# Kernel tuning notes

Hardware: AMD Instinct MI355X
Metric: run time of the kernel (lower is better)

Reference implementation:

```python
import jax, jax.numpy as jnp
import numpy as np
import math

N, C_S, C_Z, C_IPA, H, NQ, NV = 768, 384, 128, 16, 12, 4, 8


def setup_inputs() -> dict:
    key = jax.random.key(0)
    ks = jax.random.split(key, 16)
    inp = {
        "s": jax.random.normal(ks[0], (N, C_S), jnp.float32),
        "z": jax.random.normal(ks[1], (N, N, C_Z), jnp.float32),
        "rots": jax.random.normal(ks[2], (N, 3, 3), jnp.float32),
        "trans": jax.random.normal(ks[3], (N, 3), jnp.float32),
        "mask": jnp.ones((N,), jnp.float32),
    }
    sc = 0.02
    inp["Wq"] = jax.random.normal(ks[4], (C_S, H * C_IPA), jnp.float32) * sc
    inp["bq"] = jnp.zeros((H * C_IPA,), jnp.float32)
    inp["Wkv"] = jax.random.normal(ks[5], (C_S, H * 2 * C_IPA), jnp.float32) * sc
    inp["bkv"] = jnp.zeros((H * 2 * C_IPA,), jnp.float32)
    inp["Wq3"] = jax.random.normal(ks[6], (C_S, H * 3 * NQ), jnp.float32) * sc
    inp["bq3"] = jnp.zeros((H * 3 * NQ,), jnp.float32)
    inp["Wkv3"] = jax.random.normal(ks[7], (C_S, H * 3 * (NQ + NV)), jnp.float32) * sc
    inp["bkv3"] = jnp.zeros((H * 3 * (NQ + NV),), jnp.float32)
    inp["Wb"] = jax.random.normal(ks[8], (C_Z, H), jnp.float32) * sc
    inp["bb"] = jnp.zeros((H,), jnp.float32)
    inp["hw"] = jnp.zeros((H,), jnp.float32)
    inp["Wo"] = jax.random.normal(ks[9], (H * (C_Z + C_IPA + NV * 4), C_S), jnp.float32) * sc
    inp["bo"] = jnp.zeros((C_S,), jnp.float32)
    return inp


def reference(s, z, rots, trans, mask, Wq, bq, Wkv, bkv, Wq3, bq3, Wkv3, bkv3, Wb, bb, hw, Wo, bo):
    normsize = math.sqrt(1.0 / (3 * C_IPA))
    normsize_B = math.sqrt(1.0 / 3.0)
    normsize_hw = math.sqrt(1.0 / (3 * NQ * 9.0 / 2))

    # scalar Q/K/V: [N, H, C_IPA]
    Q = (s @ Wq + bq).reshape(N, H, C_IPA)
    KV = (s @ Wkv + bkv).reshape(N, H, 2, C_IPA)
    K, V = KV[..., 0, :], KV[..., 1, :]

    # query points: project, place into global frame via rigid transform
    Q3 = (s @ Wq3 + bq3).reshape(N, 3, NQ * H).swapaxes(-1, -2)        # [N, NQ*H, 3]
    Q3 = jnp.einsum('nij,nkj->nki', rots, Q3) + trans[:, None, :]
    Q3 = Q3.reshape(N, H, NQ, 3)

    KV3 = (s @ Wkv3 + bkv3).reshape(N, 3, H * (NQ + NV)).swapaxes(-1, -2)
    KV3 = jnp.einsum('nij,nkj->nki', rots, KV3) + trans[:, None, :]
    KV3 = KV3.reshape(N, H, NQ + NV, 3)
    K3, V3 = KV3[:, :, :NQ, :], KV3[:, :, NQ:, :]                      # points per head

    # pair bias [N, N, H]
    B = z @ Wb + bb

    # scalar attention logits + pair bias
    AT = jnp.einsum('ihc,jhc->ijh', Q, K) * normsize + B * normsize_B

    # point attention: squared distances [N, N, H, NQ]
    d2 = jnp.sum(jnp.square(Q3[:, None] - K3[None, :]), axis=-1)
    hw_sp = jax.nn.softplus(hw) * normsize_hw                          # [H]
    AT3 = -0.5 * jnp.sum(d2 * hw_sp[None, None, :, None], axis=-1)     # [N, N, H]

    # mask bias: large negative where either residue masked out
    mask2 = mask[:, None] * mask[None, :]
    B3 = (mask2 - 1.0) * 1e9                                           # [N, N]

    AT = jax.nn.softmax(AT + AT3 + B3[..., None], axis=-2)             # softmax over j

    # scalar value aggregation
    O = jnp.einsum('ijh,jhc->ihc', AT, V).reshape(N, -1)

    # point value aggregation, then map back to local frame (inverse transform)
    O3 = jnp.einsum('ijh,jhcd->ihcd', AT, V3).reshape(N, H * NV, 3)
    O3 = jnp.einsum('nji,nkj->nki', rots, O3 - trans[:, None, :])      # rots^T @ (O3 - t)
    O3_norm = jnp.sqrt(jnp.sum(jnp.square(O3), axis=-1) + 1e-20)       # [N, H*NV]

    # pair representation aggregation
    O_pair = jnp.einsum('ijh,ijc->ihc', AT, z).reshape(N, -1)

    O_final = jnp.concatenate((O, O3[..., 0], O3[..., 1], O3[..., 2], O3_norm, O_pair), axis=-1)
    return O_final @ Wo + bo
```

## Files before the change

kernel.cpp:

```cpp
#include <hip/hip_runtime.h>
#include <cstdint>


typedef __attribute__((ext_vector_type(8))) short short8;
typedef __attribute__((ext_vector_type(4))) short short4_t;
typedef __attribute__((ext_vector_type(4))) float f32x4;

__device__ __forceinline__ unsigned short f2bf(float f) {
    unsigned u = __float_as_uint(f);
    u = (u + 0x7FFFu + ((u >> 16) & 1u)) >> 16;
    return (unsigned short)u;
}
__device__ __forceinline__ float bf2f(unsigned short s) {
    return __uint_as_float(((unsigned)s) << 16);
}
__device__ __forceinline__ unsigned pk2(float lo, float hi) {
    return (unsigned)f2bf(lo) | ((unsigned)f2bf(hi) << 16);
}
__device__ __forceinline__ int HOFF(int gg) {
    return gg * 6 + ((gg & 2) << 2);
}

#define NS_QK  0.14433756729740643f
#define NS_B   0.5773502691896258f
#define NS_HW  0.13608276348795434f

__global__ __launch_bounds__(256) void proj_kernel(
    const float* __restrict__ s,
    const float* __restrict__ Wq,   const float* __restrict__ bq,
    const float* __restrict__ Wkv,  const float* __restrict__ bkv,
    const float* __restrict__ Wq3,  const float* __restrict__ bq3,
    const float* __restrict__ Wkv3, const float* __restrict__ bkv3,
    float* __restrict__ Qw, unsigned short* __restrict__ Kw,
    unsigned short* __restrict__ Vt,
    float* __restrict__ P3q, float* __restrict__ P3kv)
{
    __shared__ __align__(16) float s_lds[32 * 384];
    const int t  = threadIdx.x;
    const int r0 = blockIdx.x * 32;
    const int c0 = blockIdx.y * 128;

    for (int u = t; u < 3072; u += 256) {
        int r = u / 96, c4 = u - r * 96;
        *(float4*)&s_lds[r * 384 + c4 * 4] =
            *(const float4*)&s[(size_t)(r0 + r) * 384 + c4 * 4];
    }
    __syncthreads();

    const int rg = t >> 6;
    const int lc = t & 63;
    const int colA = c0 + lc;
    const int colB = c0 + lc + 64;

    const float *wpA, *wpB; int ldA, ldB; float biasA, biasB;
    {
        int col = colA;
        if (col < 192)      { wpA = Wq   + col;       ldA = 192; biasA = bq[col]; }
        else if (col < 576) { wpA = Wkv  + (col-192); ldA = 384; biasA = bkv[col-192]; }
        else if (col < 720) { wpA = Wq3  + (col-576); ldA = 144; biasA = bq3[col-576]; }
        else                { wpA = Wkv3 + (col-720); ldA = 432; biasA = bkv3[col-720]; }
        col = colB;
        if (col < 192)      { wpB = Wq   + col;       ldB = 192; biasB = bq[col]; }
        else if (col < 576) { wpB = Wkv  + (col-192); ldB = 384; biasB = bkv[col-192]; }
        else if (col < 720) { wpB = Wq3  + (col-576); ldB = 144; biasB = bq3[col-576]; }
        else                { wpB = Wkv3 + (col-720); ldB = 432; biasB = bkv3[col-720]; }
    }

    float acc0[8] = {}, acc1[8] = {};
    for (int k = 0; k < 384; k += 4) {
        float4 sv[8];
        #pragma unroll
        for (int r = 0; r < 8; r++)
            sv[r] = *(const float4*)&s_lds[(rg*8 + r) * 384 + k];
        #pragma unroll
        for (int kk = 0; kk < 4; kk++) {
            float w0 = wpA[(k + kk) * ldA];
            float w1 = wpB[(k + kk) * ldB];
            #pragma unroll
            for (int r = 0; r < 8; r++) {
                float sval = ((const float*)&sv[r])[kk];
                acc0[r] += sval * w0;
                acc1[r] += sval * w1;
            }
        }
    }

    #pragma unroll
    for (int q = 0; q < 2; q++) {
        int col   = q ? colB : colA;
        float bia = q ? biasB : biasA;
        #pragma unroll
        for (int r = 0; r < 8; r++) {
            int row = r0 + rg*8 + r;
            float v = (q ? acc1[r] : acc0[r]) + bia;
            if (col < 192) {
                Qw[(size_t)row*192 + col] = v;
            } else if (col < 576) {
                int c = col - 192, h = c >> 5, sub = c & 31;
                if (sub < 16) Kw[(size_t)row*192 + h*16 + sub] = f2bf(v);
                else          Vt[(size_t)(h*16 + (sub-16))*768 + row] = f2bf(v);
            } else if (col < 720) {
                P3q[(size_t)row*144 + (col-576)] = v;
            } else {
                P3kv[(size_t)row*432 + (col-720)] = v;
            }
        }
    }
}

__global__ __launch_bounds__(192) void rot3_kernel(
    const float* __restrict__ P3q, const float* __restrict__ P3kv,
    const float* __restrict__ rots, const float* __restrict__ trans,
    float* __restrict__ Q3w, float* __restrict__ K3w,
    unsigned short* __restrict__ V3t)
{
    const int n = blockIdx.x;
    const int t = threadIdx.x;
    float R[9];
    #pragma unroll
    for (int u = 0; u < 9; u++) R[u] = rots[n*9 + u];
    float T0 = trans[n*3+0], T1 = trans[n*3+1], T2 = trans[n*3+2];

    float p0, p1, p2;
    if (t < 48) {
        p0 = P3q[(size_t)n*144 + t];
        p1 = P3q[(size_t)n*144 + 48 + t];
        p2 = P3q[(size_t)n*144 + 96 + t];
    } else {
        int k = t - 48;
        p0 = P3kv[(size_t)n*432 + k];
        p1 = P3kv[(size_t)n*432 + 144 + k];
        p2 = P3kv[(size_t)n*432 + 288 + k];
    }
    float o0 = R[0]*p0 + R[1]*p1 + R[2]*p2 + T0;
    float o1 = R[3]*p0 + R[4]*p1 + R[5]*p2 + T1;
    float o2 = R[6]*p0 + R[7]*p1 + R[8]*p2 + T2;

    if (t < 48) {
        Q3w[(size_t)n*144 + t*3 + 0] = o0;
        Q3w[(size_t)n*144 + t*3 + 1] = o1;
        Q3w[(size_t)n*144 + t*3 + 2] = o2;
    } else {
        int k = t - 48, h = k / 12, m = k % 12;
        if (m < 4) {
            size_t base = (size_t)n*144 + (h*4 + m)*3;
            K3w[base+0] = o0; K3w[base+1] = o1; K3w[base+2] = o2;
        } else {
            int rv = (h*8 + (m-4))*3;
            V3t[(size_t)(rv+0)*768 + n] = f2bf(o0);
            V3t[(size_t)(rv+1)*768 + n] = f2bf(o1);
            V3t[(size_t)(rv+2)*768 + n] = f2bf(o2);
        }
    }
}

__global__ __launch_bounds__(256) void ek_kernel(
    const float* __restrict__ Qw, const unsigned short* __restrict__ Kw,
    const float* __restrict__ Q3w, const float* __restrict__ K3w,
    const float* __restrict__ mask, const float* __restrict__ hw,
    const float* __restrict__ bb,
    unsigned short* __restrict__ EQw, unsigned short* __restrict__ EKw)
{
    const int idx = blockIdx.x * 4 + (threadIdx.x >> 6);
    const int h   = threadIdx.x & 63;
    if (h >= 12) return;
    const float hws = log1pf(__expf(hw[h])) * NS_HW;
    const float mi  = mask[idx];
    const float S   = 31616.0f;

    unsigned short row[32];
    {
        const unsigned short* kp = Kw + (size_t)idx*192 + h*16;
        #pragma unroll
        for (int c = 0; c < 16; c++) row[c] = kp[c];
        const float* k3 = K3w + (size_t)idx*144 + h*12;
        float kn = 0.0f;
        #pragma unroll
        for (int e = 0; e < 12; e++) {
            unsigned short b = f2bf(k3[e]);
            row[16+e] = b;
            float f = bf2f(b); kn += f*f;
        }
        row[28] = f2bf(bb[h]*NS_B - 0.5f*hws*kn);
        row[29] = f2bf(1.0f);
        row[30] = f2bf(mi * S);
        row[31] = f2bf(-S);
        unsigned short* o = EKw + ((size_t)idx*12 + h)*32;
        #pragma unroll
        for (int c = 0; c < 32; c++) o[c] = row[c];
    }
    {
        const float* qp = Qw + (size_t)idx*192 + h*16;
        #pragma unroll
        for (int c = 0; c < 16; c++) row[c] = f2bf(qp[c] * NS_QK);
        const float* q3 = Q3w + (size_t)idx*144 + h*12;
        float qn = 0.0f;
        #pragma unroll
        for (int e = 0; e < 12; e++) {
            float f = q3[e];
            row[16+e] = f2bf(f * hws);
            qn += f*f;
        }
        row[28] = f2bf(1.0f);
        row[29] = f2bf(-0.5f*hws*qn);
        row[30] = f2bf(mi * S);
        row[31] = f2bf(S);
        unsigned short* o = EQw + ((size_t)idx*12 + h)*32;
        #pragma unroll
        for (int c = 0; c < 32; c++) o[c] = row[c];
    }
}

__global__ __launch_bounds__(256, 2) void ipa_main(
    const float* __restrict__ z,
    const float* __restrict__ Wb,
    const unsigned short* __restrict__ EQw, const unsigned short* __restrict__ EKw,
    const unsigned short* __restrict__ Vt, const unsigned short* __restrict__ V3t,
    float* __restrict__ part3)
{
    __shared__ __align__(16) unsigned short z_l[90 * 88];
    __shared__ __align__(16) float          p_l[2][32 * 17];
    __shared__ __align__(16) unsigned short pT_l[2][16 * 40];
    __shared__ __align__(16) float          eq_l[12 * 33];
    __shared__ __align__(16) unsigned short wbT_l[16 * 136];

    const int i     = blockIdx.x >> 1;
    const int chunk = blockIdx.x & 1;
    const int t    = threadIdx.x;
    const int lane = t & 63;
    const int wv   = t >> 6;
    const int g    = lane >> 4;
    const int lm   = lane & 15;

    for (int u = t; u < 384; u += 256) {
        int h = u >> 5, c = u & 31;
        eq_l[h*33 + c] = bf2f(EQw[((size_t)i*12 + h)*32 + c]);
    }
    for (int u = t; u < 1536; u += 256) {
        int h = u % 12, c = u / 12;
        wbT_l[h*136 + c] = f2bf(Wb[c*12 + h]);
    }
    for (int u = t; u < 512; u += 256)
        wbT_l[(12 + (u >> 7))*136 + (u & 127)] = 0;
    if (t < 160) { pT_l[0][480 + t] = 0; pT_l[1][480 + t] = 0; }

    const int jj  = t >> 3, c16 = t & 7;
    const float* zbase = z + ((size_t)i*768 + chunk*384 + jj)*128 + c16*16;
    const int chS  = (jj >> 2)*8 + c16;
    const int chP  = chS + HOFF(chS >> 4);
    const int sidx = chP*88 + (jj & 3)*16;

    f32x4 opA = {0,0,0,0}, opB = {0,0,0,0};
    float oa = 0, ob = 0, oc2 = 0;
    float o3x = 0, o3y = 0, o3z = 0;
    float dn = 0;
    const int w = t - 128;

    {
        float4 f0 = *(const float4*)(zbase + 0);
        float4 f1 = *(const float4*)(zbase + 4);
        float4 f2 = *(const float4*)(zbase + 8);
        float4 f3 = *(const float4*)(zbase + 12);
        uint4* dst = (uint4*)&z_l[sidx];
        dst[0] = uint4{pk2(f0.x,f0.y), pk2(f0.z,f0.w), pk2(f1.x,f1.y), pk2(f1.z,f1.w)};
        dst[1] = uint4{pk2(f2.x,f2.y), pk2(f2.z,f2.w), pk2(f3.x,f3.y), pk2(f3.z,f3.w)};
    }
    __syncthreads();

    auto vwork = [&](int tt) {
        const int j0v = chunk*384 + tt*32;
        const float* pp = p_l[tt & 1];
        if (w < 96) {
            const int ohp = w >> 4, o3hp = w >> 3;
            const unsigned short* vp  = Vt  + (size_t)w*768 + j0v;
            const unsigned short* v3p = V3t + (size_t)(w*3)*768 + j0v;
            #pragma unroll
            for (int q = 0; q < 4; q++) {
                short8 va = *(const short8*)(vp + q*8);
                short8 v0 = *(const short8*)(v3p + q*8);
                short8 v1 = *(const short8*)(v3p + 768 + q*8);
                short8 v2 = *(const short8*)(v3p + 1536 + q*8);
                #pragma unroll
                for (int e = 0; e < 8; e++) {
                    int j2 = q*8 + e;
                    float p1 = pp[j2*17 + ohp];
                    oa += p1 * bf2f((unsigned short)va[e]);
                    float pv = pp[j2*17 + o3hp];
                    o3x += pv * bf2f((unsigned short)v0[e]);
                    o3y += pv * bf2f((unsigned short)v1[e]);
                    o3z += pv * bf2f((unsigned short)v2[e]);
                }
            }
        } else {
            const int ha = w >> 4, hb = ha + 2, hc = ha + 4;
            const int dh = w - 96;
            const unsigned short* vp = Vt + (size_t)w*768 + j0v;
            #pragma unroll
            for (int q = 0; q < 4; q++) {
                short8 va = *(const short8*)(vp + q*8);
                short8 vb = *(const short8*)(vp + 768*32 + q*8);
                short8 vc = *(const short8*)(vp + 768*64 + q*8);
                #pragma unroll
                for (int e = 0; e < 8; e++) {
                    int j2 = q*8 + e;
                    oa  += pp[j2*17 + ha] * bf2f((unsigned short)va[e]);
                    ob  += pp[j2*17 + hb] * bf2f((unsigned short)vb[e]);
                    oc2 += pp[j2*17 + hc] * bf2f((unsigned short)vc[e]);
                }
            }
            if (dh < 12) {
                #pragma unroll
                for (int j2 = 0; j2 < 32; j2++) dn += pp[j2*17 + dh];
            }
        }
    };

    for (int tile = 0; tile < 12; tile++) {
        const int j0  = chunk*384 + tile*32;
        const int cur = tile & 1;
        const bool more = (tile < 11);

        float4 zf0, zf1, zf2, zf3;
        if (more) {
            const float* zp = zbase + (size_t)(tile + 1) * 4096;
            zf0 = *(const float4*)(zp + 0);
            zf1 = *(const float4*)(zp + 4);
            zf2 = *(const float4*)(zp + 8);
            zf3 = *(const float4*)(zp + 12);
        }

        if (wv < 2) {
            f32x4 ab = {0,0,0,0};
            #pragma unroll
            for (int ks = 0; ks < 4; ks++) {
                short8 bf = *(const short8*)&wbT_l[lm*136 + ks*32 + g*8];
                int jr = wv*16 + lm;
                int ch = (jr >> 2)*8 + ks*2 + (g >> 1);
                int cp = ch + HOFF(ch >> 4);
                short8 a = *(const short8*)&z_l[cp*88 + (jr & 3)*16 + (g & 1)*8];
                ab = __builtin_amdgcn_mfma_f32_16x16x32_bf16(a, bf, ab, 0, 0, 0);
            }
            if (lm < 12) {
                const float* eqh = eq_l + lm*33;
                #pragma unroll
                for (int r = 0; r < 4; r++) {
                    int jl = wv*16 + g*4 + r;
                    int j  = j0 + jl;
                    const unsigned short* ek = EKw + ((size_t)j*12 + lm)*32;
                    short8 e0 = *(const short8*)(ek);
                    short8 e1 = *(const short8*)(ek + 8);
                    short8 e2 = *(const short8*)(ek + 16);
                    short8 e3 = *(const short8*)(ek + 24);
                    float acc = ab[r] * NS_B;
                    #pragma unroll
                    for (int c = 0; c < 8; c++) acc += eqh[c]      * bf2f((unsigned short)e0[c]);
                    #pragma unroll
                    for (int c = 0; c < 8; c++) acc += eqh[8 + c]  * bf2f((unsigned short)e1[c]);
                    #pragma unroll
                    for (int c = 0; c < 8; c++) acc += eqh[16 + c] * bf2f((unsigned short)e2[c]);
                    #pragma unroll
                    for (int c = 0; c < 6; c++) acc += eqh[24 + c] * bf2f((unsigned short)e3[c]);
                    float mterm = eqh[30] * bf2f((unsigned short)e3[6]);
                    mterm += eqh[31] * bf2f((unsigned short)e3[7]);
                    acc += mterm;
                    float p = __expf(acc);
                    p_l[cur][jl*17 + lm]  = p;
                    pT_l[cur][lm*40 + jl] = f2bf(p);
                }
            }
        } else {
            if (tile > 0) vwork(tile - 1);
        }

        uint4 s0, s1;
        if (more) {
            s0 = uint4{pk2(zf0.x,zf0.y), pk2(zf0.z,zf0.w), pk2(zf1.x,zf1.y), pk2(zf1.z,zf1.w)};
            s1 = uint4{pk2(zf2.x,zf2.y), pk2(zf2.z,zf2.w), pk2(zf3.x,zf3.y), pk2(zf3.z,zf3.w)};
        }
        __syncthreads();

        {
            const int nt0 = wv*2;
            short8 ap = *(const short8*)((const char*)pT_l[cur] + lm*80 + g*16);
            short8 b0, b1;
            #pragma unroll
            for (int e = 0; e < 8; e++) {
                int jje = g*8 + e;
                int su  = (jje >> 2)*8;
                int ro  = (jje & 3)*16;
                int cp0 = su + nt0 + HOFF(g);
                b0[e] = (short)z_l[cp0*88 + ro + lm];
                b1[e] = (short)z_l[(cp0 + 1)*88 + ro + lm];
            }
            opA = __builtin_amdgcn_mfma_f32_16x16x32_bf16(ap, b0, opA, 0, 0, 0);
            opB = __builtin_amdgcn_mfma_f32_16x16x32_bf16(ap, b1, opB, 0, 0, 0);
        }
        __syncthreads();

        if (more) {
            uint4* dst = (uint4*)&z_l[sidx];
            dst[0] = s0; dst[1] = s1;
        }
        __syncthreads();
    }

    if (wv >= 2) vwork(11);

    float* pb = part3 + (size_t)blockIdx.x * 2560;
    if (wv >= 2) {
        pb[w] = oa;
        if (w < 96) {
            pb[192 + w*3 + 0] = o3x;
            pb[192 + w*3 + 1] = o3y;
            pb[192 + w*3 + 2] = o3z;
        } else {
            pb[w + 32] = ob;
            pb[w + 64] = oc2;
            if (w - 96 < 12) pb[2304 + (w - 96)] = dn;
        }
    }
    {
        const int nt0 = wv*2;
        #pragma unroll
        for (int r = 0; r < 4; r++) {
            int h = g*4 + r;
            if (h < 12) {
                pb[768 + h*128 + nt0*16 + lm]       = opA[r];
                pb[768 + h*128 + (nt0 + 1)*16 + lm] = opB[r];
            }
        }
    }
}

__global__ __launch_bounds__(256) void combine_kernel(
    const float* __restrict__ part3, const float* __restrict__ rots,
    const float* __restrict__ trans, unsigned short* __restrict__ OF)
{
    const int i = blockIdx.x;
    const int t = threadIdx.x;
    const float* pa = part3 + (size_t)i*2*2560;
    const float* pb = pa + 2560;
    __shared__ float den_s[12];
    if (t < 12) den_s[t] = pa[2304 + t] + pb[2304 + t];
    __syncthreads();

    const size_t ofb = (size_t)i * 2112;
    if (t < 192) OF[ofb + t] = f2bf((pa[t] + pb[t]) / den_s[t >> 4]);
    if (t < 96) {
        int h = t >> 3, v = t & 7;
        float den = den_s[h];
        int base = 192 + t*3;
        float m0 = (pa[base+0] + pb[base+0]) / den - trans[i*3+0];
        float m1 = (pa[base+1] + pb[base+1]) / den - trans[i*3+1];
        float m2 = (pa[base+2] + pb[base+2]) / den - trans[i*3+2];
        const float* R = rots + (size_t)i*9;
        float r0v = R[0]*m0 + R[3]*m1 + R[6]*m2;
        float r1v = R[1]*m0 + R[4]*m1 + R[7]*m2;
        float r2v = R[2]*m0 + R[5]*m1 + R[8]*m2;
        float nrm = sqrtf(r0v*r0v + r1v*r1v + r2v*r2v + 1e-20f);
        int hv = h*8 + v;
        OF[ofb + 192 + hv] = f2bf(r0v);
        OF[ofb + 288 + hv] = f2bf(r1v);
        OF[ofb + 384 + hv] = f2bf(r2v);
        OF[ofb + 480 + hv] = f2bf(nrm);
    }
    for (int u = t; u < 1536; u += 256) {
        OF[ofb + 576 + u] = f2bf((pa[768 + u] + pb[768 + u]) / den_s[u >> 7]);
    }
}

__global__ __launch_bounds__(256) void out_gemm(
    const unsigned short* __restrict__ OF, const float* __restrict__ Wo,
    float* __restrict__ part)
{
    __shared__ __align__(16) float aT[32 * 132];
    __shared__ __align__(16) float bt[32 * 68];
    const int t  = threadIdx.x;
    const int i0 = blockIdx.x * 128;
    const int c0 = blockIdx.y * 64;
    const int k0 = blockIdx.z * 352;
    const int r0 = (t & 15) * 8;
    const int c4 = (t >> 4) * 4;

    float acc[8][4] = {};

    for (int kt = 0; kt < 11; kt++) {
        const int kk0 = k0 + kt*32;
        __syncthreads();
        {
            int r = t >> 1, kh = (t & 1) * 16;
            const unsigned short* apg = OF + (size_t)(i0 + r)*2112 + kk0 + kh;
            short8 v0 = *(const short8*)apg;
            short8 v1 = *(const short8*)(apg + 8);
            #pragma unroll
            for (int e = 0; e < 8; e++) aT[(kh + e)*132 + r]     = bf2f((unsigned short)v0[e]);
            #pragma unroll
            for (int e = 0; e < 8; e++) aT[(kh + 8 + e)*132 + r] = bf2f((unsigned short)v1[e]);
        }
        {
            int k = t >> 3, c8 = (t & 7) * 8;
            const float* wpg = Wo + (size_t)(kk0 + k)*384 + c0 + c8;
            *(float4*)&bt[k*68 + c8]     = *(const float4*)wpg;
            *(float4*)&bt[k*68 + c8 + 4] = *(const float4*)(wpg + 4);
        }
        __syncthreads();
        #pragma unroll 4
        for (int kk = 0; kk < 32; kk++) {
            float4 a0 = *(float4*)&aT[kk*132 + r0];
            float4 a1 = *(float4*)&aT[kk*132 + r0 + 4];
            float4 bv = *(float4*)&bt[kk*68 + c4];
            #pragma unroll
            for (int ci = 0; ci < 4; ci++) {
                float b = ((const float*)&bv)[ci];
                acc[0][ci] += ((const float*)&a0)[0] * b;
                acc[1][ci] += ((const float*)&a0)[1] * b;
                acc[2][ci] += ((const float*)&a0)[2] * b;
                acc[3][ci] += ((const float*)&a0)[3] * b;
                acc[4][ci] += ((const float*)&a1)[0] * b;
                acc[5][ci] += ((const float*)&a1)[1] * b;
                acc[6][ci] += ((const float*)&a1)[2] * b;
                acc[7][ci] += ((const float*)&a1)[3] * b;
            }
        }
    }

    float* pbv = part + (size_t)blockIdx.z * 294912;
    #pragma unroll
    for (int ri = 0; ri < 8; ri++) {
        float4 o = {acc[ri][0], acc[ri][1], acc[ri][2], acc[ri][3]};
        *(float4*)&pbv[(size_t)(i0 + r0 + ri)*384 + c0 + c4] = o;
    }
}

__global__ __launch_bounds__(256) void reduce_out(
    const float* __restrict__ part, const float* __restrict__ bo,
    float* __restrict__ out)
{
    int idx = blockIdx.x * 256 + threadIdx.x;
    float v = bo[idx % 384];
    #pragma unroll
    for (int s = 0; s < 6; s++) v += part[(size_t)s * 294912 + idx];
    out[idx] = v;
}

extern "C" void kernel_launch(void* const* d_in, const int* in_sizes, int n_in,
                              void* d_out, int out_size, void* d_ws, size_t ws_size,
                              hipStream_t stream) {
    const float* s     = (const float*)d_in[0];
    const float* z     = (const float*)d_in[1];
    const float* rots  = (const float*)d_in[2];
    const float* trans = (const float*)d_in[3];
    const float* mask  = (const float*)d_in[4];
    const float* Wq    = (const float*)d_in[5];
    const float* bq    = (const float*)d_in[6];
    const float* Wkv   = (const float*)d_in[7];
    const float* bkv   = (const float*)d_in[8];
    const float* Wq3   = (const float*)d_in[9];
    const float* bq3   = (const float*)d_in[10];
    const float* Wkv3  = (const float*)d_in[11];
    const float* bkv3  = (const float*)d_in[12];
    const float* Wb    = (const float*)d_in[13];
    const float* bb    = (const float*)d_in[14];
    const float* hw    = (const float*)d_in[15];
    const float* Wo    = (const float*)d_in[16];
    const float* bo    = (const float*)d_in[17];
    float* out = (float*)d_out;

    char* ws = (char*)d_ws;
    float*          Qw   = (float*)(ws + 0);
    float*          Q3w  = (float*)(ws + 589824);
    unsigned short* Kw   = (unsigned short*)(ws + 1032192);
    unsigned short* Vt   = (unsigned short*)(ws + 1327104);
    float*          K3w  = (float*)(ws + 1622016);
    unsigned short* V3t  = (unsigned short*)(ws + 2064384);
    float*          P3q  = (float*)(ws + 2506752);
    float*          P3kv = (float*)(ws + 2949120);
    unsigned short* EQw  = (unsigned short*)(ws + 4276224);
    unsigned short* EKw  = (unsigned short*)(ws + 4866048);
    unsigned short* OF   = (unsigned short*)(ws + 5455872);
    float*          part3 = (float*)(ws + 8699904);
    float*          part  = (float*)(ws + 8699904);

    proj_kernel<<<dim3(24, 9), 256, 0, stream>>>(
        s, Wq, bq, Wkv, bkv, Wq3, bq3, Wkv3, bkv3, Qw, Kw, Vt, P3q, P3kv);
    rot3_kernel<<<768, 192, 0, stream>>>(P3q, P3kv, rots, trans, Q3w, K3w, V3t);
    ek_kernel<<<192, 256, 0, stream>>>(Qw, Kw, Q3w, K3w, mask, hw, bb, EQw, EKw);
    ipa_main<<<1536, 256, 0, stream>>>(z, Wb, EQw, EKw, Vt, V3t, part3);
    combine_kernel<<<768, 256, 0, stream>>>(part3, rots, trans, OF);
    out_gemm<<<dim3(6, 6, 6), 256, 0, stream>>>(OF, Wo, part);
    reduce_out<<<1152, 256, 0, stream>>>(part, bo, out);
}
```

Before: 307.9 us.

## Spread logit and value aggregation across all waves, drop double-buffered P tiles

The kernel previously specialised its waves: two waves computed the pair-bias MFMA plus the logits and exponentials, while the other two ran the value aggregation one tile behind on double-buffered P. Now the bias MFMA results go to a small shared buffer, all 256 threads share the logit/exp work, and every thread then does one or two value-accumulation rows for the current tile. The single-buffered P shrinks LDS use, and the launch bound asks for 3 blocks per CU. In exchange each tile gets an extra barrier, the cross-tile overlap between the two wave groups is lost, and the tighter register budget could cause spills.

```diff
diff --git a/kernel.cpp b/kernel.cpp
--- a/kernel.cpp
+++ b/kernel.cpp
@@ -211,7 +211,7 @@
     }
 }
 
-__global__ __launch_bounds__(256, 2) void ipa_main(
+__global__ __launch_bounds__(256, 3) void ipa_main(
     const float* __restrict__ z,
     const float* __restrict__ Wb,
     const unsigned short* __restrict__ EQw, const unsigned short* __restrict__ EKw,
@@ -219,8 +219,9 @@
     float* __restrict__ part3)
 {
     __shared__ __align__(16) unsigned short z_l[90 * 88];
-    __shared__ __align__(16) float          p_l[2][32 * 17];
-    __shared__ __align__(16) unsigned short pT_l[2][16 * 40];
+    __shared__ __align__(16) float          p_l[32 * 17];
+    __shared__ __align__(16) unsigned short pT_l[16 * 40];
+    __shared__ __align__(16) float          zb_l[32 * 13];
     __shared__ __align__(16) float          eq_l[12 * 33];
     __shared__ __align__(16) unsigned short wbT_l[16 * 136];
 
@@ -242,7 +243,7 @@
     }
     for (int u = t; u < 512; u += 256)
         wbT_l[(12 + (u >> 7))*136 + (u & 127)] = 0;
-    if (t < 160) { pT_l[0][480 + t] = 0; pT_l[1][480 + t] = 0; }
+    if (t < 160) pT_l[480 + t] = 0;
 
     const int jj  = t >> 3, c16 = t & 7;
     const float* zbase = z + ((size_t)i*768 + chunk*384 + jj)*128 + c16*16;
@@ -250,11 +251,16 @@
     const int chP  = chS + HOFF(chS >> 4);
     const int sidx = chP*88 + (jj & 3)*16;
 
+    const unsigned short* rp1 = (t < 192)
+        ? Vt + (size_t)t*768 : V3t + (size_t)(t - 192)*768;
+    const int h1 = (t < 192) ? (t >> 4) : ((t - 192) / 24);
+    const bool has2 = (t < 224);
+    const unsigned short* rp2 = V3t + (size_t)(t + 64)*768;
+    const int h2 = (t + 64) / 24;
+    const int denh = (t >= 224 && t < 236) ? (t - 224) : -1;
+
     f32x4 opA = {0,0,0,0}, opB = {0,0,0,0};
-    float oa = 0, ob = 0, oc2 = 0;
-    float o3x = 0, o3y = 0, o3z = 0;
-    float dn = 0;
-    const int w = t - 128;
+    float acc1 = 0, acc2 = 0, dn = 0;
 
     {
         float4 f0 = *(const float4*)(zbase + 0);
@@ -267,57 +273,8 @@
     }
     __syncthreads();
 
-    auto vwork = [&](int tt) {
-        const int j0v = chunk*384 + tt*32;
-        const float* pp = p_l[tt & 1];
-        if (w < 96) {
-            const int ohp = w >> 4, o3hp = w >> 3;
-            const unsigned short* vp  = Vt  + (size_t)w*768 + j0v;
-            const unsigned short* v3p = V3t + (size_t)(w*3)*768 + j0v;
-            #pragma unroll
-            for (int q = 0; q < 4; q++) {
-                short8 va = *(const short8*)(vp + q*8);
-                short8 v0 = *(const short8*)(v3p + q*8);
-                short8 v1 = *(const short8*)(v3p + 768 + q*8);
-                short8 v2 = *(const short8*)(v3p + 1536 + q*8);
-                #pragma unroll
-                for (int e = 0; e < 8; e++) {
-                    int j2 = q*8 + e;
-                    float p1 = pp[j2*17 + ohp];
-                    oa += p1 * bf2f((unsigned short)va[e]);
-                    float pv = pp[j2*17 + o3hp];
-                    o3x += pv * bf2f((unsigned short)v0[e]);
-                    o3y += pv * bf2f((unsigned short)v1[e]);
-                    o3z += pv * bf2f((unsigned short)v2[e]);
-                }
-            }
-        } else {
-            const int ha = w >> 4, hb = ha + 2, hc = ha + 4;
-            const int dh = w - 96;
-            const unsigned short* vp = Vt + (size_t)w*768 + j0v;
-            #pragma unroll
-            for (int q = 0; q < 4; q++) {
-                short8 va = *(const short8*)(vp + q*8);
-                short8 vb = *(const short8*)(vp + 768*32 + q*8);
-                short8 vc = *(const short8*)(vp + 768*64 + q*8);
-                #pragma unroll
-                for (int e = 0; e < 8; e++) {
-                    int j2 = q*8 + e;
-                    oa  += pp[j2*17 + ha] * bf2f((unsigned short)va[e]);
-                    ob  += pp[j2*17 + hb] * bf2f((unsigned short)vb[e]);
-                    oc2 += pp[j2*17 + hc] * bf2f((unsigned short)vc[e]);
-                }
-            }
-            if (dh < 12) {
-                #pragma unroll
-                for (int j2 = 0; j2 < 32; j2++) dn += pp[j2*17 + dh];
-            }
-        }
-    };
-
     for (int tile = 0; tile < 12; tile++) {
         const int j0  = chunk*384 + tile*32;
-        const int cur = tile & 1;
         const bool more = (tile < 11);
 
         float4 zf0, zf1, zf2, zf3;
@@ -341,47 +298,48 @@
                 ab = __builtin_amdgcn_mfma_f32_16x16x32_bf16(a, bf, ab, 0, 0, 0);
             }
             if (lm < 12) {
-                const float* eqh = eq_l + lm*33;
-                #pragma unroll
-                for (int r = 0; r < 4; r++) {
-                    int jl = wv*16 + g*4 + r;
-                    int j  = j0 + jl;
-                    const unsigned short* ek = EKw + ((size_t)j*12 + lm)*32;
-                    short8 e0 = *(const short8*)(ek);
-                    short8 e1 = *(const short8*)(ek + 8);
-                    short8 e2 = *(const short8*)(ek + 16);
-                    short8 e3 = *(const short8*)(ek + 24);
-                    float acc = ab[r] * NS_B;
-                    #pragma unroll
-                    for (int c = 0; c < 8; c++) acc += eqh[c]      * bf2f((unsigned short)e0[c]);
-                    #pragma unroll
-                    for (int c = 0; c < 8; c++) acc += eqh[8 + c]  * bf2f((unsigned short)e1[c]);
-                    #pragma unroll
-                    for (int c = 0; c < 8; c++) acc += eqh[16 + c] * bf2f((unsigned short)e2[c]);
-                    #pragma unroll
-                    for (int c = 0; c < 6; c++) acc += eqh[24 + c] * bf2f((unsigned short)e3[c]);
-                    float mterm = eqh[30] * bf2f((unsigned short)e3[6]);
-                    mterm += eqh[31] * bf2f((unsigned short)e3[7]);
-                    acc += mterm;
-                    float p = __expf(acc);
-                    p_l[cur][jl*17 + lm]  = p;
-                    pT_l[cur][lm*40 + jl] = f2bf(p);
-                }
-            }
-        } else {
-            if (tile > 0) vwork(tile - 1);
-        }
-
-        uint4 s0, s1;
-        if (more) {
-            s0 = uint4{pk2(zf0.x,zf0.y), pk2(zf0.z,zf0.w), pk2(zf1.x,zf1.y), pk2(zf1.z,zf1.w)};
-            s1 = uint4{pk2(zf2.x,zf2.y), pk2(zf2.z,zf2.w), pk2(zf3.x,zf3.y), pk2(zf3.z,zf3.w)};
+                #pragma unroll
+                for (int r = 0; r < 4; r++)
+                    zb_l[(wv*16 + g*4 + r)*13 + lm] = ab[r];
+            }
+        }
+        __syncthreads();
+
+        {
+            auto b2item = [&](int id) {
+                int jq = (id * 21846) >> 18;
+                int h  = id - jq*12;
+                float Bv = zb_l[jq*13 + h];
+                const float* eqh = eq_l + h*33;
+                const unsigned short* ek = EKw + ((size_t)(j0 + jq)*12 + h)*32;
+                short8 e0 = *(const short8*)(ek);
+                short8 e1 = *(const short8*)(ek + 8);
+                short8 e2 = *(const short8*)(ek + 16);
+                short8 e3 = *(const short8*)(ek + 24);
+                float acc = Bv * NS_B;
+                #pragma unroll
+                for (int c = 0; c < 8; c++) acc += eqh[c]      * bf2f((unsigned short)e0[c]);
+                #pragma unroll
+                for (int c = 0; c < 8; c++) acc += eqh[8 + c]  * bf2f((unsigned short)e1[c]);
+                #pragma unroll
+                for (int c = 0; c < 8; c++) acc += eqh[16 + c] * bf2f((unsigned short)e2[c]);
+                #pragma unroll
+                for (int c = 0; c < 6; c++) acc += eqh[24 + c] * bf2f((unsigned short)e3[c]);
+                float mterm = eqh[30] * bf2f((unsigned short)e3[6]);
+                mterm += eqh[31] * bf2f((unsigned short)e3[7]);
+                acc += mterm;
+                float p = __expf(acc);
+                p_l[jq*17 + h]  = p;
+                pT_l[h*40 + jq] = f2bf(p);
+            };
+            b2item(t);
+            if (t >= 128) b2item(t + 128);
         }
         __syncthreads();
 
         {
             const int nt0 = wv*2;
-            short8 ap = *(const short8*)((const char*)pT_l[cur] + lm*80 + g*16);
+            short8 ap = *(const short8*)((const char*)pT_l + lm*80 + g*16);
             short8 b0, b1;
             #pragma unroll
             for (int e = 0; e < 8; e++) {
@@ -395,6 +353,32 @@
             opA = __builtin_amdgcn_mfma_f32_16x16x32_bf16(ap, b0, opA, 0, 0, 0);
             opB = __builtin_amdgcn_mfma_f32_16x16x32_bf16(ap, b1, opB, 0, 0, 0);
         }
+        {
+            const unsigned short* r1 = rp1 + j0;
+            const unsigned short* r2 = rp2 + j0;
+            #pragma unroll
+            for (int q = 0; q < 4; q++) {
+                short8 va = *(const short8*)(r1 + q*8);
+                short8 vb;
+                if (has2) vb = *(const short8*)(r2 + q*8);
+                #pragma unroll
+                for (int e = 0; e < 8; e++) {
+                    int j2 = q*8 + e;
+                    acc1 += p_l[j2*17 + h1] * bf2f((unsigned short)va[e]);
+                    if (has2) acc2 += p_l[j2*17 + h2] * bf2f((unsigned short)vb[e]);
+                }
+            }
+            if (denh >= 0) {
+                #pragma unroll
+                for (int j2 = 0; j2 < 32; j2++) dn += p_l[j2*17 + denh];
+            }
+        }
+
+        uint4 s0, s1;
+        if (more) {
+            s0 = uint4{pk2(zf0.x,zf0.y), pk2(zf0.z,zf0.w), pk2(zf1.x,zf1.y), pk2(zf1.z,zf1.w)};
+            s1 = uint4{pk2(zf2.x,zf2.y), pk2(zf2.z,zf2.w), pk2(zf3.x,zf3.y), pk2(zf3.z,zf3.w)};
+        }
         __syncthreads();
 
         if (more) {
@@ -404,21 +388,10 @@
         __syncthreads();
     }
 
-    if (wv >= 2) vwork(11);
-
     float* pb = part3 + (size_t)blockIdx.x * 2560;
-    if (wv >= 2) {
-        pb[w] = oa;
-        if (w < 96) {
-            pb[192 + w*3 + 0] = o3x;
-            pb[192 + w*3 + 1] = o3y;
-            pb[192 + w*3 + 2] = o3z;
-        } else {
-            pb[w + 32] = ob;
-            pb[w + 64] = oc2;
-            if (w - 96 < 12) pb[2304 + (w - 96)] = dn;
-        }
-    }
+    pb[t] = acc1;
+    if (has2) pb[t + 256] = acc2;
+    if (denh >= 0) pb[2304 + denh] = dn;
     {
         const int nt0 = wv*2;
         #pragma unroll
```

Result: no change. 311.5 us (+1.2%).
